# Performance work log

Measured on AMD Instinct MI355X. Metric: run time of the kernel, lower is better.

The kernel has to match this reference:

```python
import jax, jax.numpy as jnp
import numpy as np
import math

EMBED_DIM = 512
NUM_HEADS = 8
HEAD_DIM = EMBED_DIM // NUM_HEADS
B, S = 4, 2048


def setup_inputs() -> dict:
    key = jax.random.key(0)
    ks = jax.random.split(key, 12)
    d = EMBED_DIM
    # Xavier-uniform bound for square linear layers
    bound = math.sqrt(6.0 / (d + d))
    def lin_w(k):
        return jax.random.uniform(k, (d, d), jnp.float32, -bound, bound)
    return {
        "x": jax.random.normal(ks[0], (B, S, d), jnp.float32),
        "mask": jax.random.randint(ks[1], (B, S), 0, 2) == 1,  # True = masked out
        "wq": lin_w(ks[2]), "bq": jnp.zeros((d,), jnp.float32),
        "wk": lin_w(ks[3]), "bk": jnp.zeros((d,), jnp.float32),
        "wv": lin_w(ks[4]), "bv": jnp.zeros((d,), jnp.float32),
        "wo": lin_w(ks[5]), "bo": jnp.zeros((d,), jnp.float32),
        "ln_gamma": jnp.ones((d,), jnp.float32),
        "ln_beta": jnp.zeros((d,), jnp.float32),
        "temperature": jnp.full((1,), 1.0 / math.sqrt(HEAD_DIM), jnp.float32),
    }


def _layer_norm(x, gamma, beta, eps=1e-6):
    mu = jnp.mean(x, axis=-1, keepdims=True)
    var = jnp.var(x, axis=-1, keepdims=True)
    return (x - mu) * jax.lax.rsqrt(var + eps) * gamma + beta


def reference(x, mask, wq, bq, wk, bk, wv, bv, wo, bo, ln_gamma, ln_beta, temperature):
    Bv, Sv, d = x.shape
    H, hd = NUM_HEADS, HEAD_DIM
    # torch nn.Linear: y = x @ W.T + b (W is [out, in])
    def proj(w, b):
        return (jnp.einsum("bsd,ed->bse", x, w) + b).reshape(Bv, Sv, H, hd).transpose(0, 2, 1, 3)
    q = proj(wq, bq)  # [B, H, S, hd]
    k = proj(wk, bk)
    v = proj(wv, bv)
    scores = jnp.einsum("bhqd,bhkd->bhqk", q, k) * temperature[0]  # [B,H,S,S]
    scores = jnp.where(mask[:, None, None, :], jnp.float32(-1e9), scores)
    attn = jax.nn.softmax(scores, axis=-1)  # dropout is identity in eval
    out = jnp.einsum("bhqk,bhkd->bhqd", attn, v)
    out = out.transpose(0, 2, 1, 3).reshape(Bv, Sv, d)
    out = jnp.einsum("bsd,ed->bse", out, wo) + bo
    return _layer_norm(out + x, ln_gamma, ln_beta)
```

## Files before the change

### kernel.cpp

```cpp
#include <hip/hip_runtime.h>
#include <hip/hip_bf16.h>
#include <stdint.h>

#define B_ 4
#define S_ 2048
#define D_ 512
#define H_ 8
#define HD_ 64
#define M_ (B_*S_)

typedef __bf16 bf16x8 __attribute__((ext_vector_type(8)));
typedef float f32x4 __attribute__((ext_vector_type(4)));
typedef float f32x16 __attribute__((ext_vector_type(16)));

__device__ __forceinline__ unsigned short f2b(float f) {
  union { float f; unsigned u; } v; v.f = f;
  unsigned r = v.u + 0x7fff + ((v.u >> 16) & 1);
  return (unsigned short)(r >> 16);
}

__device__ __forceinline__ float b2f(unsigned short u) {
  union { unsigned u; float f; } v; v.u = (unsigned)u << 16;
  return v.f;
}

__device__ __forceinline__ float exp2_hw(float x) {
  return __builtin_amdgcn_exp2f(x);
}

__device__ __forceinline__ unsigned cvtpk_bf16(float lo, float hi) {
  unsigned r;
  asm("v_cvt_pk_bf16_f32 %0, %1, %2" : "=v"(r) : "v"(lo), "v"(hi));
  return r;
}

__device__ __forceinline__ void plswap(unsigned &a, unsigned &b) {
  asm volatile("v_permlane32_swap_b32 %0, %1" : "+v"(a), "+v"(b));
}

__device__ __forceinline__ void gload16(const void* g, void* lds) {
  __builtin_amdgcn_global_load_lds(
      (const __attribute__((address_space(1))) unsigned int*)g,
      (__attribute__((address_space(3))) unsigned int*)lds, 16, 0, 0);
}

#define XN4 (M_ * D_ / 4)
#define WN4 (D_ * D_ / 4)
__global__ __launch_bounds__(256) void cvt_all_kernel(const float* __restrict__ x,
    const float* __restrict__ wq, const float* __restrict__ wk,
    const float* __restrict__ wv, const float* __restrict__ wo,
    unsigned short* __restrict__ xb, unsigned short* __restrict__ wqb,
    unsigned short* __restrict__ wkb, unsigned short* __restrict__ wvb,
    unsigned short* __restrict__ wob) {
  int i = blockIdx.x * blockDim.x + threadIdx.x;
  const float* src; unsigned short* dst; int off;
  if (i < XN4) { src = x; dst = xb; off = i; }
  else {
    int j = i - XN4;
    int sel = j / WN4; off = j - sel * WN4;
    src = (sel == 0) ? wq : (sel == 1) ? wk : (sel == 2) ? wv : wo;
    dst = (sel == 0) ? wqb : (sel == 1) ? wkb : (sel == 2) ? wvb : wob;
  }
  float4 v = ((const float4*)src)[off];
  ushort4 o;
  o.x = f2b(v.x); o.y = f2b(v.y); o.z = f2b(v.z); o.w = f2b(v.w);
  ((ushort4*)dst)[off] = o;
}

__device__ __forceinline__ void gemm_core_db(const unsigned short* __restrict__ A,
                                             const unsigned short* __restrict__ W,
                                             int m0, int n0, f32x4 (&acc)[4][4],
                                             unsigned short (&As)[2][128 * 64],
                                             unsigned short (&Bs)[2][128 * 64]) {
  int tid = threadIdx.x;
  int w = tid >> 6, lane = tid & 63;
  int l15 = lane & 15, g = lane >> 4;
  int wr = w >> 1, wc = w & 1;
  #define STAGE_G(buf, k0_) do {                                               \
    _Pragma("unroll")                                                          \
    for (int i = 0; i < 4; ++i) {                                              \
      int l = i * 256 + w * 64 + lane;                                         \
      int row = l >> 3, seg = l & 7;                                           \
      int sseg = seg ^ (row & 7);                                              \
      gload16(A + (size_t)(m0 + row) * D_ + (k0_) + sseg * 8,                  \
              (char*)As[buf] + (size_t)(i * 256 + w * 64) * 16);               \
      gload16(W + (size_t)(n0 + row) * D_ + (k0_) + sseg * 8,                  \
              (char*)Bs[buf] + (size_t)(i * 256 + w * 64) * 16);               \
    }                                                                          \
  } while (0)
  STAGE_G(0, 0);
  __syncthreads();
  for (int ks = 0; ks < 8; ++ks) {
    int cur = ks & 1;
    if (ks < 7) STAGE_G(cur ^ 1, (ks + 1) * 64);
    #pragma unroll
    for (int kk = 0; kk < 2; ++kk) {
      int sw = ((kk * 4 + g) ^ (l15 & 7)) * 8;
      bf16x8 af[4], bfr[4];
      #pragma unroll
      for (int t = 0; t < 4; ++t) {
        af[t]  = *(const bf16x8*)&As[cur][(wr * 64 + t * 16 + l15) * 64 + sw];
        bfr[t] = *(const bf16x8*)&Bs[cur][(wc * 64 + t * 16 + l15) * 64 + sw];
      }
      #pragma unroll
      for (int mi = 0; mi < 4; ++mi)
        #pragma unroll
        for (int ni = 0; ni < 4; ++ni)
          acc[mi][ni] = __builtin_amdgcn_mfma_f32_16x16x32_bf16(af[mi], bfr[ni], acc[mi][ni], 0, 0, 0);
    }
    __syncthreads();
  }
  #undef STAGE_G
}

__global__ __launch_bounds__(256) void gemm_qkv(const unsigned short* __restrict__ xb,
    const unsigned short* __restrict__ wqb, const unsigned short* __restrict__ wkb,
    const unsigned short* __restrict__ wvb,
    const float* __restrict__ bq, const float* __restrict__ bk, const float* __restrict__ bv,
    const float* __restrict__ tptr,
    unsigned short* __restrict__ Qb, unsigned short* __restrict__ Kb, unsigned short* __restrict__ Vtb) {
  __shared__ unsigned short As[2][128 * 64], Bs[2][128 * 64];
  int z = blockIdx.z;
  const unsigned short* W = (z == 0) ? wqb : ((z == 1) ? wkb : wvb);
  const float* bias = (z == 0) ? bq : ((z == 1) ? bk : bv);
  float scale = (z == 0) ? tptr[0] * 1.44269504088896340736f : 1.0f;
  int m0 = blockIdx.x * 128, n0 = blockIdx.y * 128;
  f32x4 zero4 = {0.f, 0.f, 0.f, 0.f};
  f32x4 acc[4][4];
  #pragma unroll
  for (int mi = 0; mi < 4; ++mi)
    #pragma unroll
    for (int ni = 0; ni < 4; ++ni) acc[mi][ni] = zero4;
  gemm_core_db(xb, W, m0, n0, acc, As, Bs);
  int tid = threadIdx.x;
  int w = tid >> 6, lane = tid & 63, l15 = lane & 15, g = lane >> 4;
  int wr = w >> 1, wc = w & 1;
  if (z == 2) {
    unsigned short* T = &As[0][0];
    #pragma unroll
    for (int mi = 0; mi < 4; ++mi)
      #pragma unroll
      for (int ni = 0; ni < 4; ++ni) {
        int el = wc * 64 + ni * 16 + l15;
        float bb = bias[n0 + el];
        int sx = (el & 15) << 3;
        #pragma unroll
        for (int r = 0; r < 4; ++r) {
          int s = wr * 64 + mi * 16 + g * 4 + r;
          T[el * 128 + (s ^ sx)] = f2b(acc[mi][ni][r] + bb);
        }
      }
    __syncthreads();
    int el = tid >> 1, hf = tid & 1;
    int eg = n0 + el, h = eg >> 6, dd = eg & 63;
    int bI = m0 >> 11, sbase = (m0 & 2047) + hf * 64;
    unsigned short* dst = &Vtb[((size_t)(bI * H_ + h) * HD_ + dd) * S_ + sbase];
    const unsigned short* srcR = &T[el * 128];
    int j = el & 15;
    #pragma unroll
    for (int c = 0; c < 8; ++c) {
      int cc = (hf * 8 + c) ^ j;
      uint4 v = *(const uint4*)&srcR[cc * 8];
      *(uint4*)&dst[c * 8] = v;
    }
  } else {
    #pragma unroll
    for (int mi = 0; mi < 4; ++mi)
      #pragma unroll
      for (int ni = 0; ni < 4; ++ni) {
        int e = n0 + wc * 64 + ni * 16 + l15;
        float bb = bias[e];
        int h = e >> 6, dd = e & 63;
        #pragma unroll
        for (int r = 0; r < 4; ++r) {
          int m = m0 + wr * 64 + mi * 16 + g * 4 + r;
          int b = m >> 11, s = m & 2047;
          unsigned short u = f2b((acc[mi][ni][r] + bb) * scale);
          int bh = b * H_ + h;
          if (z == 0) Qb[((size_t)bh * S_ + s) * HD_ + dd] = u;
          else        Kb[((size_t)bh * S_ + s) * HD_ + dd] = u;
        }
      }
  }
}

__global__ __launch_bounds__(256) void gemm_proj(const unsigned short* __restrict__ AOb,
    const unsigned short* __restrict__ wob, const float* __restrict__ bo,
    unsigned short* __restrict__ Pfb) {
  __shared__ unsigned short As[2][128 * 64], Bs[2][128 * 64];
  int m0 = blockIdx.x * 128, n0 = blockIdx.y * 128;
  f32x4 zero4 = {0.f, 0.f, 0.f, 0.f};
  f32x4 acc[4][4];
  #pragma unroll
  for (int mi = 0; mi < 4; ++mi)
    #pragma unroll
    for (int ni = 0; ni < 4; ++ni) acc[mi][ni] = zero4;
  gemm_core_db(AOb, wob, m0, n0, acc, As, Bs);
  int tid = threadIdx.x;
  int w = tid >> 6, lane = tid & 63, l15 = lane & 15, g = lane >> 4;
  int wr = w >> 1, wc = w & 1;
  #pragma unroll
  for (int mi = 0; mi < 4; ++mi)
    #pragma unroll
    for (int ni = 0; ni < 4; ++ni) {
      int e = n0 + wc * 64 + ni * 16 + l15;
      float bb = bo[e];
      #pragma unroll
      for (int r = 0; r < 4; ++r) {
        int m = m0 + wr * 64 + mi * 16 + g * 4 + r;
        Pfb[(size_t)m * D_ + e] = f2b(acc[mi][ni][r] + bb);
      }
    }
}

__global__ __launch_bounds__(256, 2) void attn_kernel(const unsigned short* __restrict__ Qb,
    const unsigned short* __restrict__ Kb, const unsigned short* __restrict__ Vtb,
    const int* __restrict__ mask, unsigned short* __restrict__ AOb) {
  __shared__ unsigned short Ks[3][64 * 64], Vs[3][64 * 64];
  __shared__ uint4 mlds[32][4][2];
  int bid = blockIdx.y * gridDim.x + blockIdx.x;
  int xcd = bid & 7, j = bid >> 3;
  int bh = xcd * 4 + (j >> 4);
  int qblk = j & 15;
  int b = bh >> 3, h = bh & 7;
  int tid = threadIdx.x, w = tid >> 6, lane = tid & 63;
  int l31 = lane & 31, hi = lane >> 5;
  int q0w = qblk * 128 + w * 32;
  const unsigned short* Qbase = Qb + (size_t)bh * S_ * HD_;
  const int* mbase = mask + (size_t)b * S_;

  bf16x8 qf[4];
  #pragma unroll
  for (int kk = 0; kk < 4; ++kk)
    qf[kk] = *(const bf16x8*)&Qbase[(size_t)(q0w + l31) * HD_ + kk * 16 + hi * 8];

  bf16x8 ones;
  #pragma unroll
  for (int jj = 0; jj < 8; ++jj) ones[jj] = (__bf16)1.0f;

  f32x16 out[2], lacc, zc;
  #pragma unroll
  for (int i = 0; i < 16; ++i) { out[0][i] = 0.f; out[1][i] = 0.f; lacc[i] = 0.f; zc[i] = 0.f; }

  f32x16 stA[2], stB[2];

  #define STAGE_KV(buf, kb_) do {                                              \
    _Pragma("unroll")                                                          \
    for (int i = 0; i < 2; ++i) {                                              \
      int l = i * 256 + w * 64 + lane;                                         \
      int row = l >> 3, seg = l & 7;                                           \
      int sseg = seg ^ (row & 7);                                              \
      gload16(Kb + ((size_t)bh * S_ + (kb_) + row) * HD_ + sseg * 8,           \
              (char*)Ks[buf] + (size_t)(i * 256 + w * 64) * 16);               \
      gload16(Vtb + ((size_t)bh * HD_ + row) * S_ + (kb_) + sseg * 8,          \
              (char*)Vs[buf] + (size_t)(i * 256 + w * 64) * 16);               \
    }                                                                          \
  } while (0)

  #define QKT_TILE(KSBUF, ST) do {                                             \
    __builtin_amdgcn_s_setprio(1);                                             \
    const unsigned short* kbase_ = Ks[KSBUF];                                  \
    _Pragma("unroll")                                                          \
    for (int kk = 0; kk < 4; ++kk) {                                           \
      int sw = ((2 * kk + hi) ^ (l31 & 7)) * 8;                                \
      bf16x8 ka0 = *(const bf16x8*)&kbase_[l31 * 64 + sw];                     \
      bf16x8 ka1 = *(const bf16x8*)&kbase_[(32 + l31) * 64 + sw];              \
      ST[0] = __builtin_amdgcn_mfma_f32_32x32x16_bf16(ka0, qf[kk], kk ? ST[0] : zc, 0, 0, 0); \
      ST[1] = __builtin_amdgcn_mfma_f32_32x32x16_bf16(ka1, qf[kk], kk ? ST[1] : zc, 0, 0, 0); \
    }                                                                          \
    __builtin_amdgcn_s_setprio(0);                                             \
  } while (0)

  #define TILE_BODY(T, STC, STN, bPV, bQK, bST) do {                           \
    __syncthreads();                                                           \
    if ((T) + 2 < 32) STAGE_KV(bST, ((T) + 2) * 64);                           \
    if ((T) + 1 < 32) QKT_TILE(bQK, STN);                                      \
    _Pragma("unroll")                                                          \
    for (int ktile = 0; ktile < 2; ++ktile)                                    \
      _Pragma("unroll")                                                        \
      for (int reg = 0; reg < 16; ++reg)                                       \
        STC[ktile][reg] = exp2_hw(STC[ktile][reg]);                            \
    __builtin_amdgcn_s_setprio(1);                                             \
    const unsigned short* vbase_ = Vs[bPV];                                    \
    _Pragma("unroll")                                                          \
    for (int kp = 0; kp < 4; ++kp) {                                           \
      const int kt8 = kp >> 1;                                                 \
      const int ro = 8 * (kp & 1);                                             \
      uint4 mw = mlds[(T)][kp][hi];                                            \
      unsigned Xa = cvtpk_bf16(STC[kt8][ro + 0], STC[kt8][ro + 1]);            \
      unsigned Ya = cvtpk_bf16(STC[kt8][ro + 4], STC[kt8][ro + 5]);            \
      unsigned Xb = cvtpk_bf16(STC[kt8][ro + 2], STC[kt8][ro + 3]);            \
      unsigned Yb = cvtpk_bf16(STC[kt8][ro + 6], STC[kt8][ro + 7]);            \
      plswap(Xa, Ya);                                                          \
      plswap(Xb, Yb);                                                          \
      union { unsigned u[4]; bf16x8 v; } pu;                                   \
      pu.u[0] = Xa & mw.x; pu.u[1] = Xb & mw.y;                                \
      pu.u[2] = Ya & mw.z; pu.u[3] = Yb & mw.w;                                \
      bf16x8 pa = pu.v;                                                        \
      _Pragma("unroll")                                                        \
      for (int dn = 0; dn < 2; ++dn) {                                         \
        int row = dn * 32 + l31;                                               \
        bf16x8 vb = *(const bf16x8*)&vbase_[row * 64 + ((2 * kp + hi) ^ (row & 7)) * 8]; \
        out[dn] = __builtin_amdgcn_mfma_f32_32x32x16_bf16(pa, vb, out[dn], 0, 0, 0); \
      }                                                                        \
      lacc = __builtin_amdgcn_mfma_f32_32x32x16_bf16(pa, ones, lacc, 0, 0, 0); \
    }                                                                          \
    __builtin_amdgcn_s_setprio(0);                                             \
  } while (0)

  STAGE_KV(0, 0);
  {
    int t = tid;
    int tile = t >> 3, kp = (t >> 1) & 3, hh = t & 1;
    const int* mp = mbase + tile * 64 + kp * 16 + hh * 8;
    uint4 mw;
    mw.x = (mp[0] ? 0u : 0x0000FFFFu) | (mp[1] ? 0u : 0xFFFF0000u);
    mw.y = (mp[2] ? 0u : 0x0000FFFFu) | (mp[3] ? 0u : 0xFFFF0000u);
    mw.z = (mp[4] ? 0u : 0x0000FFFFu) | (mp[5] ? 0u : 0xFFFF0000u);
    mw.w = (mp[6] ? 0u : 0x0000FFFFu) | (mp[7] ? 0u : 0xFFFF0000u);
    mlds[tile][kp][hh] = mw;
  }
  __syncthreads();
  STAGE_KV(1, 64);
  QKT_TILE(0, stA);

  int b0 = 0, b1 = 1, b2 = 2;
  for (int tp = 0; tp < 16; ++tp) {
    int t = 2 * tp;
    TILE_BODY(t, stA, stB, b0, b1, b2);
    TILE_BODY(t + 1, stB, stA, b1, b2, b0);
    int btmp = b0; b0 = b2; b2 = b1; b1 = btmp;
  }

  #pragma unroll
  for (int reg = 0; reg < 16; ++reg) {
    float inv = 1.f / lacc[reg];
    int q = q0w + (reg & 3) + 8 * (reg >> 2) + 4 * hi;
    #pragma unroll
    for (int dn = 0; dn < 2; ++dn)
      AOb[((size_t)b * S_ + q) * D_ + h * HD_ + dn * 32 + l31] = f2b(out[dn][reg] * inv);
  }
  #undef TILE_BODY
  #undef QKT_TILE
  #undef STAGE_KV
}

__global__ __launch_bounds__(256) void ln_kernel(const unsigned short* __restrict__ Pfb,
    const float* __restrict__ x, const float* __restrict__ gamma,
    const float* __restrict__ beta, float* __restrict__ out) {
  int row = blockIdx.x * 4 + (threadIdx.x >> 6);
  int lane = threadIdx.x & 63;
  const unsigned short* pr = Pfb + (size_t)row * D_;
  const float* xr = x + (size_t)row * D_;
  ushort4 p0 = *(const ushort4*)(pr + lane * 8);
  ushort4 p1 = *(const ushort4*)(pr + lane * 8 + 4);
  float4 b0 = *(const float4*)(xr + lane * 8);
  float4 b1 = *(const float4*)(xr + lane * 8 + 4);
  float y[8] = {b2f(p0.x) + b0.x, b2f(p0.y) + b0.y, b2f(p0.z) + b0.z, b2f(p0.w) + b0.w,
                b2f(p1.x) + b1.x, b2f(p1.y) + b1.y, b2f(p1.z) + b1.z, b2f(p1.w) + b1.w};
  float s = 0.f, s2 = 0.f;
  #pragma unroll
  for (int i = 0; i < 8; ++i) { s += y[i]; s2 += y[i] * y[i]; }
  #pragma unroll
  for (int d = 1; d < 64; d <<= 1) { s += __shfl_xor(s, d); s2 += __shfl_xor(s2, d); }
  float mu = s * (1.f / 512.f);
  float var = s2 * (1.f / 512.f) - mu * mu;
  float inv = rsqrtf(fmaxf(var, 0.f) + 1e-6f);
  float4 g0 = *(const float4*)(gamma + lane * 8);
  float4 g1 = *(const float4*)(gamma + lane * 8 + 4);
  float4 e0 = *(const float4*)(beta + lane * 8);
  float4 e1 = *(const float4*)(beta + lane * 8 + 4);
  float* orow = out + (size_t)row * D_;
  float4 o0 = {(y[0] - mu) * inv * g0.x + e0.x, (y[1] - mu) * inv * g0.y + e0.y,
               (y[2] - mu) * inv * g0.z + e0.z, (y[3] - mu) * inv * g0.w + e0.w};
  float4 o1 = {(y[4] - mu) * inv * g1.x + e1.x, (y[5] - mu) * inv * g1.y + e1.y,
               (y[6] - mu) * inv * g1.z + e1.z, (y[7] - mu) * inv * g1.w + e1.w};
  *(float4*)(orow + lane * 8) = o0;
  *(float4*)(orow + lane * 8 + 4) = o1;
}

extern "C" void kernel_launch(void* const* d_in, const int* in_sizes, int n_in,
                              void* d_out, int out_size, void* d_ws, size_t ws_size,
                              hipStream_t stream) {
  const float* x = (const float*)d_in[0];
  const int* mask = (const int*)d_in[1];
  const float* wq = (const float*)d_in[2];
  const float* bq = (const float*)d_in[3];
  const float* wk = (const float*)d_in[4];
  const float* bk = (const float*)d_in[5];
  const float* wv = (const float*)d_in[6];
  const float* bv = (const float*)d_in[7];
  const float* wo = (const float*)d_in[8];
  const float* bo = (const float*)d_in[9];
  const float* gamma = (const float*)d_in[10];
  const float* beta = (const float*)d_in[11];
  const float* temp = (const float*)d_in[12];
  float* out = (float*)d_out;
  char* ws = (char*)d_ws;
  const size_t MB = (size_t)1 << 20;
  unsigned short* xb  = (unsigned short*)(ws);
  unsigned short* wqb = (unsigned short*)(ws + 8 * MB);
  unsigned short* wkb = (unsigned short*)(ws + 8 * MB + 512 * 1024);
  unsigned short* wvb = (unsigned short*)(ws + 9 * MB);
  unsigned short* wob = (unsigned short*)(ws + 9 * MB + 512 * 1024);
  unsigned short* Qb  = (unsigned short*)(ws + 10 * MB);
  unsigned short* Kb  = (unsigned short*)(ws + 18 * MB);
  unsigned short* Pfb = (unsigned short*)(ws + 10 * MB);
  unsigned short* Vtb = (unsigned short*)(ws + 26 * MB);
  unsigned short* AOb = (unsigned short*)(ws + 34 * MB);

  cvt_all_kernel<<<(XN4 + 4 * WN4 + 255) / 256, 256, 0, stream>>>(
      x, wq, wk, wv, wo, xb, wqb, wkb, wvb, wob);
  gemm_qkv<<<dim3(64, 4, 3), 256, 0, stream>>>(xb, wqb, wkb, wvb, bq, bk, bv, temp, Qb, Kb, Vtb);
  attn_kernel<<<dim3(16, 32), 256, 0, stream>>>(Qb, Kb, Vtb, mask, AOb);
  gemm_proj<<<dim3(64, 4), 256, 0, stream>>>(AOb, wob, bo, Pfb);
  ln_kernel<<<2048, 256, 0, stream>>>(Pfb, x, gamma, beta, out);
}
```

Measured before the change: 101.9 us.

## Compact unmasked keys and values so attention skips masked key tiles

```diff
diff --git a/kernel.cpp b/kernel.cpp
--- a/kernel.cpp
+++ b/kernel.cpp
@@ -65,6 +65,55 @@
   ushort4 o;
   o.x = f2b(v.x); o.y = f2b(v.y); o.z = f2b(v.z); o.w = f2b(v.w);
   ((ushort4*)dst)[off] = o;
+}
+
+__global__ __launch_bounds__(64) void rank_kernel(const int* __restrict__ mask,
+    int* __restrict__ idx, int* __restrict__ nkbuf) {
+  int b = blockIdx.x, lane = threadIdx.x;
+  const int* mb = mask + (size_t)b * S_;
+  int base = 0;
+  for (int c = 0; c < 32; ++c) {
+    int s = c * 64 + lane;
+    int m = mb[s];
+    unsigned long long keep = __ballot(m == 0);
+    int my = base + __popcll(keep & ((1ull << lane) - 1ull));
+    if (m == 0) idx[(size_t)b * S_ + my] = s;
+    base += __popcll(keep);
+  }
+  if (lane == 0) nkbuf[b] = base;
+}
+
+__global__ __launch_bounds__(256) void compact_kernel(const unsigned short* __restrict__ Kb,
+    const unsigned short* __restrict__ Vtb, const int* __restrict__ idx,
+    const int* __restrict__ nkbuf,
+    unsigned short* __restrict__ Kc, unsigned short* __restrict__ Vtc) {
+  int bh = blockIdx.y, b = bh >> 3;
+  int nk = nkbuf[b];
+  const int* ib = idx + (size_t)b * S_;
+  int tid = threadIdx.x;
+  if (blockIdx.z == 0) {
+    int j = blockIdx.x * 32 + (tid >> 3), ch = tid & 7;
+    if (j < nk) {
+      int s = ib[j];
+      const uint4* src = (const uint4*)&Kb[((size_t)bh * S_ + s) * HD_];
+      uint4* dst = (uint4*)&Kc[((size_t)bh * S_ + j) * HD_];
+      dst[ch] = src[ch];
+    }
+  } else {
+    int d = blockIdx.x;
+    const unsigned short* src = &Vtb[((size_t)bh * HD_ + d) * S_];
+    unsigned short* dst = &Vtc[((size_t)bh * HD_ + d) * S_];
+    int j0 = tid * 8;
+    if (j0 < nk) {
+      unsigned short tmp[8];
+      #pragma unroll
+      for (int c = 0; c < 8; ++c) {
+        int j = j0 + c;
+        tmp[c] = (j < nk) ? src[ib[j]] : (unsigned short)0;
+      }
+      *(uint4*)&dst[j0] = *(uint4*)tmp;
+    }
+  }
 }
 
 __device__ __forceinline__ void gemm_core_db(const unsigned short* __restrict__ A,
@@ -214,20 +263,21 @@
 }
 
 __global__ __launch_bounds__(256, 2) void attn_kernel(const unsigned short* __restrict__ Qb,
-    const unsigned short* __restrict__ Kb, const unsigned short* __restrict__ Vtb,
-    const int* __restrict__ mask, unsigned short* __restrict__ AOb) {
+    const unsigned short* __restrict__ Kc, const unsigned short* __restrict__ Vtc,
+    const int* __restrict__ nkbuf, unsigned short* __restrict__ AOb) {
   __shared__ unsigned short Ks[3][64 * 64], Vs[3][64 * 64];
   __shared__ uint4 mlds[32][4][2];
   int bid = blockIdx.y * gridDim.x + blockIdx.x;
-  int xcd = bid & 7, j = bid >> 3;
-  int bh = xcd * 4 + (j >> 4);
-  int qblk = j & 15;
+  int xcd = bid & 7, jj = bid >> 3;
+  int bh = xcd * 4 + (jj >> 4);
+  int qblk = jj & 15;
   int b = bh >> 3, h = bh & 7;
   int tid = threadIdx.x, w = tid >> 6, lane = tid & 63;
   int l31 = lane & 31, hi = lane >> 5;
   int q0w = qblk * 128 + w * 32;
   const unsigned short* Qbase = Qb + (size_t)bh * S_ * HD_;
-  const int* mbase = mask + (size_t)b * S_;
+  int nk = nkbuf[b];
+  int nt = (nk + 63) >> 6;
 
   bf16x8 qf[4];
   #pragma unroll
@@ -236,7 +286,7 @@
 
   bf16x8 ones;
   #pragma unroll
-  for (int jj = 0; jj < 8; ++jj) ones[jj] = (__bf16)1.0f;
+  for (int c = 0; c < 8; ++c) ones[c] = (__bf16)1.0f;
 
   f32x16 out[2], lacc, zc;
   #pragma unroll
@@ -250,9 +300,9 @@
       int l = i * 256 + w * 64 + lane;                                         \
       int row = l >> 3, seg = l & 7;                                           \
       int sseg = seg ^ (row & 7);                                              \
-      gload16(Kb + ((size_t)bh * S_ + (kb_) + row) * HD_ + sseg * 8,           \
+      gload16(Kc + ((size_t)bh * S_ + (kb_) + row) * HD_ + sseg * 8,           \
               (char*)Ks[buf] + (size_t)(i * 256 + w * 64) * 16);               \
-      gload16(Vtb + ((size_t)bh * HD_ + row) * S_ + (kb_) + sseg * 8,          \
+      gload16(Vtc + ((size_t)bh * HD_ + row) * S_ + (kb_) + sseg * 8,          \
               (char*)Vs[buf] + (size_t)(i * 256 + w * 64) * 16);               \
     }                                                                          \
   } while (0)
@@ -273,8 +323,8 @@
 
   #define TILE_BODY(T, STC, STN, bPV, bQK, bST) do {                           \
     __syncthreads();                                                           \
-    if ((T) + 2 < 32) STAGE_KV(bST, ((T) + 2) * 64);                           \
-    if ((T) + 1 < 32) QKT_TILE(bQK, STN);                                      \
+    if ((T) + 2 < nt) STAGE_KV(bST, ((T) + 2) * 64);                           \
+    if ((T) + 1 < nt) QKT_TILE(bQK, STN);                                      \
     _Pragma("unroll")                                                          \
     for (int ktile = 0; ktile < 2; ++ktile)                                    \
       _Pragma("unroll")                                                        \
@@ -312,25 +362,24 @@
   {
     int t = tid;
     int tile = t >> 3, kp = (t >> 1) & 3, hh = t & 1;
-    const int* mp = mbase + tile * 64 + kp * 16 + hh * 8;
+    int j0 = tile * 64 + kp * 16 + hh * 8;
     uint4 mw;
-    mw.x = (mp[0] ? 0u : 0x0000FFFFu) | (mp[1] ? 0u : 0xFFFF0000u);
-    mw.y = (mp[2] ? 0u : 0x0000FFFFu) | (mp[3] ? 0u : 0xFFFF0000u);
-    mw.z = (mp[4] ? 0u : 0x0000FFFFu) | (mp[5] ? 0u : 0xFFFF0000u);
-    mw.w = (mp[6] ? 0u : 0x0000FFFFu) | (mp[7] ? 0u : 0xFFFF0000u);
+    mw.x = ((j0 + 0 < nk) ? 0x0000FFFFu : 0u) | ((j0 + 1 < nk) ? 0xFFFF0000u : 0u);
+    mw.y = ((j0 + 2 < nk) ? 0x0000FFFFu : 0u) | ((j0 + 3 < nk) ? 0xFFFF0000u : 0u);
+    mw.z = ((j0 + 4 < nk) ? 0x0000FFFFu : 0u) | ((j0 + 5 < nk) ? 0xFFFF0000u : 0u);
+    mw.w = ((j0 + 6 < nk) ? 0x0000FFFFu : 0u) | ((j0 + 7 < nk) ? 0xFFFF0000u : 0u);
     mlds[tile][kp][hh] = mw;
   }
   __syncthreads();
-  STAGE_KV(1, 64);
+  if (nt > 1) STAGE_KV(1, 64);
   QKT_TILE(0, stA);
 
-  int b0 = 0, b1 = 1, b2 = 2;
-  for (int tp = 0; tp < 16; ++tp) {
-    int t = 2 * tp;
-    TILE_BODY(t, stA, stB, b0, b1, b2);
-    TILE_BODY(t + 1, stB, stA, b1, b2, b0);
-    int btmp = b0; b0 = b2; b2 = b1; b1 = btmp;
-  }
+  int t = 0;
+  for (; t + 1 < nt; t += 2) {
+    TILE_BODY(t, stA, stB, t % 3, (t + 1) % 3, (t + 2) % 3);
+    TILE_BODY(t + 1, stB, stA, (t + 1) % 3, (t + 2) % 3, t % 3);
+  }
+  if (t < nt) TILE_BODY(t, stA, stB, t % 3, (t + 1) % 3, (t + 2) % 3);
 
   #pragma unroll
   for (int reg = 0; reg < 16; ++reg) {
@@ -408,11 +457,17 @@
   unsigned short* Pfb = (unsigned short*)(ws + 10 * MB);
   unsigned short* Vtb = (unsigned short*)(ws + 26 * MB);
   unsigned short* AOb = (unsigned short*)(ws + 34 * MB);
+  unsigned short* Kc  = (unsigned short*)(ws + 42 * MB);
+  unsigned short* Vtc = (unsigned short*)(ws + 50 * MB);
+  int*            idx = (int*)(ws + 58 * MB);
+  int*            nkb = (int*)(ws + 58 * MB + 64 * 1024);
 
   cvt_all_kernel<<<(XN4 + 4 * WN4 + 255) / 256, 256, 0, stream>>>(
       x, wq, wk, wv, wo, xb, wqb, wkb, wvb, wob);
+  rank_kernel<<<4, 64, 0, stream>>>(mask, idx, nkb);
   gemm_qkv<<<dim3(64, 4, 3), 256, 0, stream>>>(xb, wqb, wkb, wvb, bq, bk, bv, temp, Qb, Kb, Vtb);
-  attn_kernel<<<dim3(16, 32), 256, 0, stream>>>(Qb, Kb, Vtb, mask, AOb);
+  compact_kernel<<<dim3(64, 32, 2), 256, 0, stream>>>(Kb, Vtb, idx, nkb, Kc, Vtc);
+  attn_kernel<<<dim3(16, 32), 256, 0, stream>>>(Qb, Kc, Vtc, nkb, AOb);
   gemm_proj<<<dim3(64, 4), 256, 0, stream>>>(AOb, wob, bo, Pfb);
   ln_kernel<<<2048, 256, 0, stream>>>(Pfb, x, gamma, beta, out);
 }
```

New measurement: 105.5 us. +3.6%, slower.
